# Optimization experiments

Measured on AMD Instinct MI355X. Metric: run time of the kernel, lower is better.

The kernel has to match this reference:

```python
import jax, jax.numpy as jnp
import numpy as np

D_MODEL = 1024
EXPANSION = 4
NUM_TILES = 4
D_FF = D_MODEL * EXPANSION


def setup_inputs() -> dict:
    key = jax.random.key(0)
    k1, k2, k3, k4, k5 = jax.random.split(key, 5)
    x = jax.random.normal(k1, (8, 2048, D_MODEL), dtype=jnp.float32)
    w_up = jax.random.normal(k2, (D_FF, D_MODEL), dtype=jnp.float32) * 0.02
    b_up = jax.random.normal(k3, (D_FF,), dtype=jnp.float32) * 0.02
    w_down = jax.random.normal(k4, (D_MODEL, D_FF), dtype=jnp.float32) * 0.02
    b_down = jax.random.normal(k5, (D_MODEL,), dtype=jnp.float32) * 0.02
    return {"x": x, "w_up": w_up, "b_up": b_up, "w_down": w_down, "b_down": b_down}


def reference(x, w_up, b_up, w_down, b_down):
    B, T, C = x.shape
    xf = x.reshape(B * T, C)  # [N, d_model]
    N = B * T

    # Emergent tile signatures: sign of per-tile row sums of up_proj weight.
    tile_up = D_FF // NUM_TILES
    signatures = jnp.sign(w_up.reshape(NUM_TILES, tile_up, C).sum(axis=1))  # [num_tiles, d_model]

    # Routing: argmax over input-signature alignment -> one-hot gate.
    scores = xf @ signatures.T                      # [N, num_tiles]
    winner = jnp.argmax(scores, axis=-1)            # [N]
    gate = jax.nn.one_hot(winner, NUM_TILES, dtype=xf.dtype)  # [N, num_tiles]

    # Tile-gated up projection (gate scales output tile blocks), then ReLU.
    hidden = xf @ w_up.T + b_up                     # [N, d_ff]
    hidden = (hidden.reshape(N, NUM_TILES, tile_up) * gate[:, :, None]).reshape(N, D_FF)
    hidden = jax.nn.relu(hidden)

    # Tile-gated down projection.
    tile_down = D_MODEL // NUM_TILES
    out = hidden @ w_down.T + b_down                # [N, d_model]
    out = (out.reshape(N, NUM_TILES, tile_down) * gate[:, :, None]).reshape(N, D_MODEL)

    return out.reshape(B, T, D_MODEL), gate.reshape(B, T, NUM_TILES)
```

## Files before the change

kernel.cpp:

```cpp
#include <hip/hip_runtime.h>
#include <stdint.h>
#include <stddef.h>

#define N_TOK 16384
#define DM    1024
#define DFF   4096
#define NT    4
#define TU    1024
#define TD    256

typedef __attribute__((ext_vector_type(8))) short  short8;
typedef __attribute__((ext_vector_type(4))) short  short4v;
typedef __attribute__((ext_vector_type(4))) float  floatx4;

__device__ inline unsigned short f2bf(float f){
  union { float f; uint32_t u; } v; v.f = f;
  uint32_t u = v.u + 0x7FFFu + ((v.u >> 16) & 1u);
  return (unsigned short)(u >> 16);
}

__device__ __forceinline__ void gll16(const void* g, void* l){
  __builtin_amdgcn_global_load_lds(
      (const __attribute__((address_space(1))) unsigned int*)g,
      (__attribute__((address_space(3))) unsigned int*)l,
      16, 0, 0);
}

__global__ void k_sig_partial(const float* __restrict__ w_up,
                              float* __restrict__ partial,
                              unsigned short* __restrict__ wupb){
  const int b = blockIdx.x, tid = threadIdx.x;
  const int tile = b >> 6, chunk = b & 63;
  const int c0 = tid * 4;
  const int row0 = tile*TU + chunk*16;
  float s0=0.f, s1=0.f, s2=0.f, s3=0.f;
  const float* base = w_up + (size_t)row0 * DM + c0;
  #pragma unroll
  for (int r = 0; r < 16; ++r){
    floatx4 v = *(const floatx4*)(base + (size_t)r * DM);
    s0 += v[0]; s1 += v[1]; s2 += v[2]; s3 += v[3];
    short4v p;
    p[0]=(short)f2bf(v[0]); p[1]=(short)f2bf(v[1]);
    p[2]=(short)f2bf(v[2]); p[3]=(short)f2bf(v[3]);
    *(short4v*)(wupb + (size_t)(row0 + r) * DM + c0) = p;
  }
  float* p = partial + ((size_t)tile*DM + c0) * 64 + chunk;
  p[0] = s0; p[64] = s1; p[128] = s2; p[192] = s3;
}

__global__ void k_sig_final(const float* __restrict__ partial,
                            float* __restrict__ sig){
  const int g = blockIdx.x * 256 + threadIdx.x;
  const float* p = partial + (size_t)g * 64;
  float s = 0.f;
  #pragma unroll
  for (int i = 0; i < 64; ++i) s += p[i];
  sig[g] = (s > 0.f) ? 1.f : ((s < 0.f) ? -1.f : 0.f);
}

__global__ void k_wdown_conv(const float* __restrict__ w,
                             unsigned short* __restrict__ wb){
  const size_t i = ((size_t)blockIdx.x * 256 + threadIdx.x) * 8;
  floatx4 v0 = *(const floatx4*)(w + i);
  floatx4 v1 = *(const floatx4*)(w + i + 4);
  short8 p;
  p[0]=(short)f2bf(v0[0]); p[1]=(short)f2bf(v0[1]); p[2]=(short)f2bf(v0[2]); p[3]=(short)f2bf(v0[3]);
  p[4]=(short)f2bf(v1[0]); p[5]=(short)f2bf(v1[1]); p[6]=(short)f2bf(v1[2]); p[7]=(short)f2bf(v1[3]);
  *(short8*)(wb + i) = p;
}

__global__ __launch_bounds__(256) void k_route(
    const float* __restrict__ x, const float* __restrict__ sig,
    float* __restrict__ gate_out, int* __restrict__ winner,
    unsigned short* __restrict__ xbf){
  __shared__ float ssig[NT * DM];
  const int tid = threadIdx.x;
  for (int i = tid; i < NT*DM; i += 256) ssig[i] = sig[i];
  __syncthreads();
  const int wv = tid >> 6, lane = tid & 63;
  const int n = blockIdx.x * 4 + wv;
  const float* xr = x + (size_t)n * DM;
  unsigned short* xb = xbf + (size_t)n * 2048 + 1024;
  double a0=0.0, a1=0.0, a2=0.0, a3=0.0;
  #pragma unroll
  for (int j = 0; j < 4; ++j){
    const int c = j*256 + lane*4;
    floatx4 v = *(const floatx4*)(xr + c);
    short4v p;
    p[0]=(short)f2bf(v[0]); p[1]=(short)f2bf(v[1]);
    p[2]=(short)f2bf(v[2]); p[3]=(short)f2bf(v[3]);
    *(short4v*)(xb + c) = p;
    #pragma unroll
    for (int u = 0; u < 4; ++u){
      double xv = (double)v[u];
      a0 += xv * (double)ssig[c+u];
      a1 += xv * (double)ssig[DM   + c+u];
      a2 += xv * (double)ssig[2*DM + c+u];
      a3 += xv * (double)ssig[3*DM + c+u];
    }
  }
  #pragma unroll
  for (int off = 32; off > 0; off >>= 1){
    a0 += __shfl_down(a0, off, 64);
    a1 += __shfl_down(a1, off, 64);
    a2 += __shfl_down(a2, off, 64);
    a3 += __shfl_down(a3, off, 64);
  }
  if (lane == 0){
    double s[4] = {a0, a1, a2, a3};
    int w = 0;
    #pragma unroll
    for (int t = 1; t < 4; ++t) if (s[t] > s[w]) w = t;
    floatx4 g = { w==0 ? 1.f:0.f, w==1 ? 1.f:0.f, w==2 ? 1.f:0.f, w==3 ? 1.f:0.f };
    *(floatx4*)(gate_out + (size_t)n * 4) = g;
    winner[n] = w;
  }
}

__global__ void k_hist(const int* __restrict__ winner,
                       int* __restrict__ blk_cnt){
  __shared__ int wcnt[4][NT];
  const int tid = threadIdx.x, wv = tid >> 6, lane = tid & 63;
  const int w = winner[blockIdx.x * 256 + tid];
  #pragma unroll
  for (int t = 0; t < NT; ++t){
    unsigned long long m = __ballot(w == t);
    if (lane == 0) wcnt[wv][t] = __popcll(m);
  }
  __syncthreads();
  if (tid < NT){
    int s = wcnt[0][tid] + wcnt[1][tid] + wcnt[2][tid] + wcnt[3][tid];
    blk_cnt[blockIdx.x * NT + tid] = s;
  }
}

__global__ void k_scan(const int* __restrict__ blk_cnt,
                       int* __restrict__ meta, int* __restrict__ blk_base){
  __shared__ int s[256];
  const int tid = threadIdx.x;
  s[tid] = blk_cnt[tid];
  __syncthreads();
  if (tid == 0){
    int tot[NT] = {0,0,0,0};
    for (int b = 0; b < 64; ++b)
      for (int t = 0; t < NT; ++t) tot[t] += s[b*NT + t];
    int off = 0, base[NT];
    for (int t = 0; t < NT; ++t){ meta[t] = tot[t]; meta[4+t] = off; base[t] = off; off += tot[t]; }
    for (int b = 0; b < 64; ++b)
      for (int t = 0; t < NT; ++t){ int c = s[b*NT + t]; s[b*NT + t] = base[t]; base[t] += c; }
  }
  __syncthreads();
  blk_base[tid] = s[tid];
}

__global__ void k_scatter(const int* __restrict__ winner,
                          const int* __restrict__ blk_base,
                          int* __restrict__ idx){
  __shared__ int wcnt[4][NT];
  const int tid = threadIdx.x, wv = tid >> 6, lane = tid & 63;
  const int n = blockIdx.x * 256 + tid;
  const int w = winner[n];
  unsigned long long mymask = 0;
  #pragma unroll
  for (int t = 0; t < NT; ++t){
    unsigned long long m = __ballot(w == t);
    if (lane == 0) wcnt[wv][t] = __popcll(m);
    if (t == w) mymask = m;
  }
  __syncthreads();
  const unsigned long long below = (lane == 0) ? 0ull : (~0ull >> (64 - lane));
  int pos = blk_base[blockIdx.x * NT + w] + __popcll(mymask & below);
  for (int v = 0; v < wv; ++v) pos += wcnt[v][w];
  idx[pos] = n;
}

__global__ __launch_bounds__(256, 2) void k_gemm1(
    const unsigned short* __restrict__ xbf,
    const unsigned short* __restrict__ wupb,
    const float* __restrict__ b_up, const int* __restrict__ meta,
    const int* __restrict__ idx, unsigned short* __restrict__ hid){
  const int tile = blockIdx.z;
  const int cnt  = meta[tile];
  const int p0   = blockIdx.x * 128;
  if (p0 >= cnt) return;
  const int off  = meta[4 + tile];
  const int nb   = blockIdx.y;

  __shared__ unsigned short smem[16384];
  unsigned short* As0 = smem;
  unsigned short* As1 = smem + 4096;
  unsigned short* Bs0 = smem + 8192;
  unsigned short* Bs1 = smem + 12288;
  __shared__ int nrow[128];

  const int tid = threadIdx.x;
  if (tid < 128){
    int p = p0 + tid;
    nrow[tid] = idx[off + (p < cnt ? p : cnt - 1)];
  }
  __syncthreads();

  const int wv = tid >> 6, lane = tid & 63;
  const int wm = (wv >> 1) * 64, wn = (wv & 1) * 64;
  const int l16 = lane & 15, quad = lane >> 4;

  const int rsub = lane >> 2;
  const int kus  = (lane & 3) * 8;

  const int ra = wv*32 + rsub;
  const unsigned short* aptr0 = xbf + (size_t)nrow[ra]      * 2048 + 1024 + kus;
  const unsigned short* aptr1 = xbf + (size_t)nrow[ra + 16] * 2048 + 1024 + kus;
  const unsigned short* bptr0 = wupb + (size_t)(tile*TU + nb*128 + wv*32 + rsub) * DM + kus;
  const unsigned short* bptr1 = bptr0 + 16 * DM;

  unsigned short* a0d0 = As0 + (wv*32) * 32;  unsigned short* a0d1 = a0d0 + 16*32;
  unsigned short* a1d0 = As1 + (wv*32) * 32;  unsigned short* a1d1 = a1d0 + 16*32;
  unsigned short* b0d0 = Bs0 + (wv*32) * 32;  unsigned short* b0d1 = b0d0 + 16*32;
  unsigned short* b1d0 = Bs1 + (wv*32) * 32;  unsigned short* b1d1 = b1d0 + 16*32;

  floatx4 acc[4][4];
  #pragma unroll
  for (int i = 0; i < 4; ++i)
    #pragma unroll
    for (int j = 0; j < 4; ++j) acc[i][j] = (floatx4){0.f,0.f,0.f,0.f};

  for (int k0 = 0; k0 < DM; k0 += 64){
    gll16(aptr0 + k0,      a0d0);
    gll16(aptr1 + k0,      a0d1);
    gll16(aptr0 + k0 + 32, a1d0);
    gll16(aptr1 + k0 + 32, a1d1);
    gll16(bptr0 + k0,      b0d0);
    gll16(bptr1 + k0,      b0d1);
    gll16(bptr0 + k0 + 32, b1d0);
    gll16(bptr1 + k0 + 32, b1d1);
    __syncthreads();
    {
      short8 af[4], bfr[4];
      #pragma unroll
      for (int i = 0; i < 4; ++i) af[i]  = *(const short8*)(As0 + (wm + i*16 + l16)*32 + quad*8);
      #pragma unroll
      for (int j = 0; j < 4; ++j) bfr[j] = *(const short8*)(Bs0 + (wn + j*16 + l16)*32 + quad*8);
      #pragma unroll
      for (int i = 0; i < 4; ++i)
        #pragma unroll
        for (int j = 0; j < 4; ++j)
          acc[i][j] = __builtin_amdgcn_mfma_f32_16x16x32_bf16(af[i], bfr[j], acc[i][j], 0, 0, 0);
    }
    {
      short8 af[4], bfr[4];
      #pragma unroll
      for (int i = 0; i < 4; ++i) af[i]  = *(const short8*)(As1 + (wm + i*16 + l16)*32 + quad*8);
      #pragma unroll
      for (int j = 0; j < 4; ++j) bfr[j] = *(const short8*)(Bs1 + (wn + j*16 + l16)*32 + quad*8);
      #pragma unroll
      for (int i = 0; i < 4; ++i)
        #pragma unroll
        for (int j = 0; j < 4; ++j)
          acc[i][j] = __builtin_amdgcn_mfma_f32_16x16x32_bf16(af[i], bfr[j], acc[i][j], 0, 0, 0);
    }
    __syncthreads();
  }

  const int gcol0 = nb*128;
  #pragma unroll
  for (int half = 0; half < 2; ++half){
    if ((wv >> 1) == half){
      #pragma unroll
      for (int i = 0; i < 4; ++i){
        #pragma unroll
        for (int j = 0; j < 4; ++j){
          const int col = wn + j*16 + l16;
          const float bias = b_up[tile*TU + gcol0 + col];
          #pragma unroll
          for (int r = 0; r < 4; ++r){
            const int lrow = i*16 + quad*4 + r;
            float v = acc[i][j][r] + bias;
            smem[lrow*136 + col] = f2bf(v > 0.f ? v : 0.f);
          }
        }
      }
    }
    __syncthreads();
    #pragma unroll
    for (int c = tid; c < 1024; c += 256){
      const int lrow = c >> 4, k8 = (c & 15) * 8;
      const int m = half*64 + lrow;
      if (p0 + m < cnt){
        short8 vv = *(const short8*)(smem + lrow*136 + k8);
        *(short8*)(hid + (size_t)nrow[m]*2048 + gcol0 + k8) = vv;
      }
    }
    __syncthreads();
  }
}

__global__ __launch_bounds__(256, 2) void k_gemm2(
    const unsigned short* __restrict__ hid,
    const unsigned short* __restrict__ wdownb,
    const float* __restrict__ b_down, const int* __restrict__ meta,
    const int* __restrict__ idx, float* __restrict__ out){
  const int tile = blockIdx.z;
  const int cnt  = meta[tile];
  const int p0   = blockIdx.x * 32;
  if (p0 >= cnt) return;
  const int off  = meta[4 + tile];

  __shared__ unsigned short smem[18432];
  unsigned short* As0 = smem;
  unsigned short* As1 = smem + 1024;
  unsigned short* Bs0 = smem + 2048;
  unsigned short* Bs1 = smem + 10240;
  float* epi = (float*)smem;
  __shared__ int nrow[32];

  const int tid = threadIdx.x;
  if (tid < 32){
    int p = p0 + tid;
    nrow[tid] = idx[off + (p < cnt ? p : cnt - 1)];
  }
  __syncthreads();

  const int wv = tid >> 6, lane = tid & 63;
  const int wn = wv * 64;
  const int l16 = lane & 15, quad = lane >> 4;

  const int rsub = lane >> 2;
  const int kus  = (lane & 3) * 8;

  const int arow = (wv & 1)*16 + rsub;
  const unsigned short* aptr = hid + (size_t)nrow[arow] * 2048 + kus;
  const int aoff = (wv >> 1) * 32;
  unsigned short* asd = (wv < 2 ? As0 : As1) + ((wv & 1)*16) * 32;
  const unsigned short* bptr = wdownb + (size_t)(tile*TD + wv*64 + rsub) * DFF + tile*TU + kus;
  unsigned short* bsd0 = Bs0 + (wv*64) * 32;
  unsigned short* bsd1 = Bs1 + (wv*64) * 32;

  floatx4 acc[2][4];
  #pragma unroll
  for (int i = 0; i < 2; ++i)
    #pragma unroll
    for (int j = 0; j < 4; ++j) acc[i][j] = (floatx4){0.f,0.f,0.f,0.f};

  for (int k0 = 0; k0 < TU; k0 += 64){
    gll16(aptr + k0 + aoff, asd);
    gll16(bptr + k0,               bsd0);
    gll16(bptr + k0 + 16*DFF,      bsd0 + 16*32);
    gll16(bptr + k0 + 32*DFF,      bsd0 + 32*32);
    gll16(bptr + k0 + 48*DFF,      bsd0 + 48*32);
    gll16(bptr + k0 + 32,          bsd1);
    gll16(bptr + k0 + 32 + 16*DFF, bsd1 + 16*32);
    gll16(bptr + k0 + 32 + 32*DFF, bsd1 + 32*32);
    gll16(bptr + k0 + 32 + 48*DFF, bsd1 + 48*32);
    __syncthreads();
    {
      short8 af[2], bfr[4];
      #pragma unroll
      for (int i = 0; i < 2; ++i) af[i]  = *(const short8*)(As0 + (i*16 + l16)*32 + quad*8);
      #pragma unroll
      for (int j = 0; j < 4; ++j) bfr[j] = *(const short8*)(Bs0 + (wn + j*16 + l16)*32 + quad*8);
      #pragma unroll
      for (int i = 0; i < 2; ++i)
        #pragma unroll
        for (int j = 0; j < 4; ++j)
          acc[i][j] = __builtin_amdgcn_mfma_f32_16x16x32_bf16(af[i], bfr[j], acc[i][j], 0, 0, 0);
    }
    {
      short8 af[2], bfr[4];
      #pragma unroll
      for (int i = 0; i < 2; ++i) af[i]  = *(const short8*)(As1 + (i*16 + l16)*32 + quad*8);
      #pragma unroll
      for (int j = 0; j < 4; ++j) bfr[j] = *(const short8*)(Bs1 + (wn + j*16 + l16)*32 + quad*8);
      #pragma unroll
      for (int i = 0; i < 2; ++i)
        #pragma unroll
        for (int j = 0; j < 4; ++j)
          acc[i][j] = __builtin_amdgcn_mfma_f32_16x16x32_bf16(af[i], bfr[j], acc[i][j], 0, 0, 0);
    }
    __syncthreads();
  }

  const floatx4 z4 = {0.f, 0.f, 0.f, 0.f};
  #pragma unroll
  for (int cb = 0; cb < 4; ++cb){
    if (cb == tile) continue;
    for (int c = tid; c < 32*64; c += 256){
      const int rowl = c >> 6, c4 = (c & 63) * 4;
      if (p0 + rowl < cnt)
        *(floatx4*)(out + (size_t)nrow[rowl]*DM + cb*256 + c4) = z4;
    }
  }

  #pragma unroll
  for (int half = 0; half < 2; ++half){
    #pragma unroll
    for (int j = 0; j < 4; ++j){
      const int col = wn + j*16 + l16;
      const float bias = b_down[tile*TD + col];
      #pragma unroll
      for (int r = 0; r < 4; ++r){
        const int lrow = quad*4 + r;
        epi[lrow*260 + col] = acc[half][j][r] + bias;
      }
    }
    __syncthreads();
    #pragma unroll
    for (int c = tid; c < 1024; c += 256){
      const int lrow = c >> 6, c4 = (c & 63) * 4;
      const int m = half*16 + lrow;
      if (p0 + m < cnt){
        floatx4 v = *(const floatx4*)(epi + lrow*260 + c4);
        *(floatx4*)(out + (size_t)nrow[m]*DM + tile*TD + c4) = v;
      }
    }
    __syncthreads();
  }
}

extern "C" void kernel_launch(void* const* d_in, const int* in_sizes, int n_in,
                              void* d_out, int out_size, void* d_ws, size_t ws_size,
                              hipStream_t stream){
  const float* x      = (const float*)d_in[0];
  const float* w_up   = (const float*)d_in[1];
  const float* b_up   = (const float*)d_in[2];
  const float* w_down = (const float*)d_in[3];
  const float* b_down = (const float*)d_in[4];

  unsigned short* wupb   = (unsigned short*)d_ws;
  unsigned short* wdownb = wupb + (size_t)DFF * DM;
  float* partial = (float*)(wdownb + (size_t)DM * DFF);
  float* sig     = partial + 262144;
  int*   ints    = (int*)(sig + 4096);
  int*   winner   = ints;
  int*   idx      = ints + 16384;
  int*   meta     = ints + 32768;
  int*   blk_cnt  = ints + 32776;
  int*   blk_base = ints + 33032;

  float*          out  = (float*)d_out;
  float*          gate = out + (size_t)N_TOK * DM;
  unsigned short* ob16 = (unsigned short*)d_out;

  k_sig_partial<<<dim3(NT*64), 256, 0, stream>>>(w_up, partial, wupb);
  k_sig_final  <<<dim3(16),    256, 0, stream>>>(partial, sig);
  k_wdown_conv <<<dim3(2048),  256, 0, stream>>>(w_down, wdownb);
  k_route      <<<dim3(N_TOK/4), 256, 0, stream>>>(x, sig, gate, winner, ob16);
  k_hist       <<<dim3(64),    256, 0, stream>>>(winner, blk_cnt);
  k_scan       <<<dim3(1),     256, 0, stream>>>(blk_cnt, meta, blk_base);
  k_scatter    <<<dim3(64),    256, 0, stream>>>(winner, blk_base, idx);
  k_gemm1      <<<dim3(128, 8, NT), 256, 0, stream>>>(ob16, wupb, b_up, meta, idx, ob16);
  k_gemm2      <<<dim3(512, 1, NT), 256, 0, stream>>>(ob16, wdownb, b_down, meta, idx, out);
}
```

Measured before the change: 273.5 us.

## Double-buffer LDS tiles in both GEMM kernels to overlap loads with MFMA

Both grouped GEMM kernels move from a load-sync-compute-sync loop to a two-stage ping-pong pipeline. The next K-slice is issued with global_load_lds into the second LDS buffer while MFMAs run on the current one. A manual vmcnt wait and s_barrier replace __syncthreads. This is meant to hide global-load latency, and in exchange it doubles LDS use (64KB and 72KB per block), which can lower occupancy below the two blocks per CU that launch_bounds targets.

```diff
diff --git a/kernel.cpp b/kernel.cpp
--- a/kernel.cpp
+++ b/kernel.cpp
@@ -186,11 +186,7 @@
   const int off  = meta[4 + tile];
   const int nb   = blockIdx.y;
 
-  __shared__ unsigned short smem[16384];
-  unsigned short* As0 = smem;
-  unsigned short* As1 = smem + 4096;
-  unsigned short* Bs0 = smem + 8192;
-  unsigned short* Bs1 = smem + 12288;
+  __shared__ unsigned short smem[32768];
   __shared__ int nrow[128];
 
   const int tid = threadIdx.x;
@@ -213,10 +209,7 @@
   const unsigned short* bptr0 = wupb + (size_t)(tile*TU + nb*128 + wv*32 + rsub) * DM + kus;
   const unsigned short* bptr1 = bptr0 + 16 * DM;
 
-  unsigned short* a0d0 = As0 + (wv*32) * 32;  unsigned short* a0d1 = a0d0 + 16*32;
-  unsigned short* a1d0 = As1 + (wv*32) * 32;  unsigned short* a1d1 = a1d0 + 16*32;
-  unsigned short* b0d0 = Bs0 + (wv*32) * 32;  unsigned short* b0d1 = b0d0 + 16*32;
-  unsigned short* b1d0 = Bs1 + (wv*32) * 32;  unsigned short* b1d1 = b1d0 + 16*32;
+  unsigned short* d0 = smem + (wv*32) * 32;
 
   floatx4 acc[4][4];
   #pragma unroll
@@ -224,22 +217,27 @@
     #pragma unroll
     for (int j = 0; j < 4; ++j) acc[i][j] = (floatx4){0.f,0.f,0.f,0.f};
 
-  for (int k0 = 0; k0 < DM; k0 += 64){
-    gll16(aptr0 + k0,      a0d0);
-    gll16(aptr1 + k0,      a0d1);
-    gll16(aptr0 + k0 + 32, a1d0);
-    gll16(aptr1 + k0 + 32, a1d1);
-    gll16(bptr0 + k0,      b0d0);
-    gll16(bptr1 + k0,      b0d1);
-    gll16(bptr0 + k0 + 32, b1d0);
-    gll16(bptr1 + k0 + 32, b1d1);
-    __syncthreads();
+  auto stage = [&](int B, int k0){
+    unsigned short* d = d0 + B*16384;
+    gll16(aptr0 + k0,      d);
+    gll16(aptr1 + k0,      d + 512);
+    gll16(aptr0 + k0 + 32, d + 4096);
+    gll16(aptr1 + k0 + 32, d + 4608);
+    gll16(bptr0 + k0,      d + 8192);
+    gll16(bptr1 + k0,      d + 8704);
+    gll16(bptr0 + k0 + 32, d + 12288);
+    gll16(bptr1 + k0 + 32, d + 12800);
+  };
+
+  auto compute = [&](int B){
+    const unsigned short* A  = smem + B*16384;
+    const unsigned short* Bp = A + 8192;
     {
       short8 af[4], bfr[4];
       #pragma unroll
-      for (int i = 0; i < 4; ++i) af[i]  = *(const short8*)(As0 + (wm + i*16 + l16)*32 + quad*8);
-      #pragma unroll
-      for (int j = 0; j < 4; ++j) bfr[j] = *(const short8*)(Bs0 + (wn + j*16 + l16)*32 + quad*8);
+      for (int i = 0; i < 4; ++i) af[i]  = *(const short8*)(A  + (wm + i*16 + l16)*32 + quad*8);
+      #pragma unroll
+      for (int j = 0; j < 4; ++j) bfr[j] = *(const short8*)(Bp + (wn + j*16 + l16)*32 + quad*8);
       #pragma unroll
       for (int i = 0; i < 4; ++i)
         #pragma unroll
@@ -249,16 +247,30 @@
     {
       short8 af[4], bfr[4];
       #pragma unroll
-      for (int i = 0; i < 4; ++i) af[i]  = *(const short8*)(As1 + (wm + i*16 + l16)*32 + quad*8);
-      #pragma unroll
-      for (int j = 0; j < 4; ++j) bfr[j] = *(const short8*)(Bs1 + (wn + j*16 + l16)*32 + quad*8);
+      for (int i = 0; i < 4; ++i) af[i]  = *(const short8*)(A  + 4096 + (wm + i*16 + l16)*32 + quad*8);
+      #pragma unroll
+      for (int j = 0; j < 4; ++j) bfr[j] = *(const short8*)(Bp + 4096 + (wn + j*16 + l16)*32 + quad*8);
       #pragma unroll
       for (int i = 0; i < 4; ++i)
         #pragma unroll
         for (int j = 0; j < 4; ++j)
           acc[i][j] = __builtin_amdgcn_mfma_f32_16x16x32_bf16(af[i], bfr[j], acc[i][j], 0, 0, 0);
     }
-    __syncthreads();
+  };
+
+  stage(0, 0);
+  asm volatile("s_waitcnt vmcnt(0)" ::: "memory");
+  __builtin_amdgcn_s_barrier();
+
+  for (int it = 0; it < 16; it += 2){
+    stage(1, (it+1)*64);
+    compute(0);
+    asm volatile("s_waitcnt vmcnt(0)" ::: "memory");
+    __builtin_amdgcn_s_barrier();
+    if (it < 14) stage(0, (it+2)*64);
+    compute(1);
+    asm volatile("s_waitcnt vmcnt(0)" ::: "memory");
+    __builtin_amdgcn_s_barrier();
   }
 
   const int gcol0 = nb*128;
@@ -305,11 +317,7 @@
   if (p0 >= cnt) return;
   const int off  = meta[4 + tile];
 
-  __shared__ unsigned short smem[18432];
-  unsigned short* As0 = smem;
-  unsigned short* As1 = smem + 1024;
-  unsigned short* Bs0 = smem + 2048;
-  unsigned short* Bs1 = smem + 10240;
+  __shared__ unsigned short smem[36864];
   float* epi = (float*)smem;
   __shared__ int nrow[32];
 
@@ -330,10 +338,10 @@
   const int arow = (wv & 1)*16 + rsub;
   const unsigned short* aptr = hid + (size_t)nrow[arow] * 2048 + kus;
   const int aoff = (wv >> 1) * 32;
-  unsigned short* asd = (wv < 2 ? As0 : As1) + ((wv & 1)*16) * 32;
+  unsigned short* asd0 = smem + (wv < 2 ? 0 : 1024) + ((wv & 1)*16) * 32;
   const unsigned short* bptr = wdownb + (size_t)(tile*TD + wv*64 + rsub) * DFF + tile*TU + kus;
-  unsigned short* bsd0 = Bs0 + (wv*64) * 32;
-  unsigned short* bsd1 = Bs1 + (wv*64) * 32;
+  unsigned short* bsd0 = smem + 2048  + (wv*64) * 32;
+  unsigned short* bsd1 = smem + 10240 + (wv*64) * 32;
 
   floatx4 acc[2][4];
   #pragma unroll
@@ -341,23 +349,29 @@
     #pragma unroll
     for (int j = 0; j < 4; ++j) acc[i][j] = (floatx4){0.f,0.f,0.f,0.f};
 
-  for (int k0 = 0; k0 < TU; k0 += 64){
-    gll16(aptr + k0 + aoff, asd);
-    gll16(bptr + k0,               bsd0);
-    gll16(bptr + k0 + 16*DFF,      bsd0 + 16*32);
-    gll16(bptr + k0 + 32*DFF,      bsd0 + 32*32);
-    gll16(bptr + k0 + 48*DFF,      bsd0 + 48*32);
-    gll16(bptr + k0 + 32,          bsd1);
-    gll16(bptr + k0 + 32 + 16*DFF, bsd1 + 16*32);
-    gll16(bptr + k0 + 32 + 32*DFF, bsd1 + 32*32);
-    gll16(bptr + k0 + 32 + 48*DFF, bsd1 + 48*32);
-    __syncthreads();
+  auto stage = [&](int B, int k0){
+    unsigned short* a  = asd0 + B*18432;
+    unsigned short* b0 = bsd0 + B*18432;
+    unsigned short* b1 = bsd1 + B*18432;
+    gll16(aptr + k0 + aoff,        a);
+    gll16(bptr + k0,               b0);
+    gll16(bptr + k0 + 16*DFF,      b0 + 512);
+    gll16(bptr + k0 + 32*DFF,      b0 + 1024);
+    gll16(bptr + k0 + 48*DFF,      b0 + 1536);
+    gll16(bptr + k0 + 32,          b1);
+    gll16(bptr + k0 + 32 + 16*DFF, b1 + 512);
+    gll16(bptr + k0 + 32 + 32*DFF, b1 + 1024);
+    gll16(bptr + k0 + 32 + 48*DFF, b1 + 1536);
+  };
+
+  auto compute = [&](int B){
+    const unsigned short* base = smem + B*18432;
     {
       short8 af[2], bfr[4];
       #pragma unroll
-      for (int i = 0; i < 2; ++i) af[i]  = *(const short8*)(As0 + (i*16 + l16)*32 + quad*8);
-      #pragma unroll
-      for (int j = 0; j < 4; ++j) bfr[j] = *(const short8*)(Bs0 + (wn + j*16 + l16)*32 + quad*8);
+      for (int i = 0; i < 2; ++i) af[i]  = *(const short8*)(base + (i*16 + l16)*32 + quad*8);
+      #pragma unroll
+      for (int j = 0; j < 4; ++j) bfr[j] = *(const short8*)(base + 2048 + (wn + j*16 + l16)*32 + quad*8);
       #pragma unroll
       for (int i = 0; i < 2; ++i)
         #pragma unroll
@@ -367,16 +381,30 @@
     {
       short8 af[2], bfr[4];
       #pragma unroll
-      for (int i = 0; i < 2; ++i) af[i]  = *(const short8*)(As1 + (i*16 + l16)*32 + quad*8);
-      #pragma unroll
-      for (int j = 0; j < 4; ++j) bfr[j] = *(const short8*)(Bs1 + (wn + j*16 + l16)*32 + quad*8);
+      for (int i = 0; i < 2; ++i) af[i]  = *(const short8*)(base + 1024 + (i*16 + l16)*32 + quad*8);
+      #pragma unroll
+      for (int j = 0; j < 4; ++j) bfr[j] = *(const short8*)(base + 10240 + (wn + j*16 + l16)*32 + quad*8);
       #pragma unroll
       for (int i = 0; i < 2; ++i)
         #pragma unroll
         for (int j = 0; j < 4; ++j)
           acc[i][j] = __builtin_amdgcn_mfma_f32_16x16x32_bf16(af[i], bfr[j], acc[i][j], 0, 0, 0);
     }
-    __syncthreads();
+  };
+
+  stage(0, 0);
+  asm volatile("s_waitcnt vmcnt(0)" ::: "memory");
+  __builtin_amdgcn_s_barrier();
+
+  for (int it = 0; it < 16; it += 2){
+    stage(1, (it+1)*64);
+    compute(0);
+    asm volatile("s_waitcnt vmcnt(0)" ::: "memory");
+    __builtin_amdgcn_s_barrier();
+    if (it < 14) stage(0, (it+2)*64);
+    compute(1);
+    asm volatile("s_waitcnt vmcnt(0)" ::: "memory");
+    __builtin_amdgcn_s_barrier();
   }
 
   const floatx4 z4 = {0.f, 0.f, 0.f, 0.f};
```

Result: slower. 291.3 us (+6.5%).

## Triple-buffer GEMM1 LDS loads with vmcnt-based async prefetch pipeline

Applied to the files above, without the earlier changes.

Replaces the load-sync-compute-sync loop in the up-projection GEMM with a 3-stage ring buffer in LDS. Global-to-LDS loads for stage s+2 are issued before computing stage s, and explicit s_waitcnt vmcnt tracks completion so loads overlap the MFMA work. This hides memory latency at the cost of more LDS per block (48KB vs 32KB), which may limit occupancy, and adds a fully unrolled loop of 32 iterations.

```diff
diff --git a/kernel.cpp b/kernel.cpp
--- a/kernel.cpp
+++ b/kernel.cpp
@@ -186,11 +186,7 @@
   const int off  = meta[4 + tile];
   const int nb   = blockIdx.y;
 
-  __shared__ unsigned short smem[16384];
-  unsigned short* As0 = smem;
-  unsigned short* As1 = smem + 4096;
-  unsigned short* Bs0 = smem + 8192;
-  unsigned short* Bs1 = smem + 12288;
+  __shared__ unsigned short smem[24576];
   __shared__ int nrow[128];
 
   const int tid = threadIdx.x;
@@ -213,52 +209,50 @@
   const unsigned short* bptr0 = wupb + (size_t)(tile*TU + nb*128 + wv*32 + rsub) * DM + kus;
   const unsigned short* bptr1 = bptr0 + 16 * DM;
 
-  unsigned short* a0d0 = As0 + (wv*32) * 32;  unsigned short* a0d1 = a0d0 + 16*32;
-  unsigned short* a1d0 = As1 + (wv*32) * 32;  unsigned short* a1d1 = a1d0 + 16*32;
-  unsigned short* b0d0 = Bs0 + (wv*32) * 32;  unsigned short* b0d1 = b0d0 + 16*32;
-  unsigned short* b1d0 = Bs1 + (wv*32) * 32;  unsigned short* b1d1 = b1d0 + 16*32;
-
   floatx4 acc[4][4];
   #pragma unroll
   for (int i = 0; i < 4; ++i)
     #pragma unroll
     for (int j = 0; j < 4; ++j) acc[i][j] = (floatx4){0.f,0.f,0.f,0.f};
 
-  for (int k0 = 0; k0 < DM; k0 += 64){
-    gll16(aptr0 + k0,      a0d0);
-    gll16(aptr1 + k0,      a0d1);
-    gll16(aptr0 + k0 + 32, a1d0);
-    gll16(aptr1 + k0 + 32, a1d1);
-    gll16(bptr0 + k0,      b0d0);
-    gll16(bptr1 + k0,      b0d1);
-    gll16(bptr0 + k0 + 32, b1d0);
-    gll16(bptr1 + k0 + 32, b1d1);
-    __syncthreads();
-    {
-      short8 af[4], bfr[4];
-      #pragma unroll
-      for (int i = 0; i < 4; ++i) af[i]  = *(const short8*)(As0 + (wm + i*16 + l16)*32 + quad*8);
-      #pragma unroll
-      for (int j = 0; j < 4; ++j) bfr[j] = *(const short8*)(Bs0 + (wn + j*16 + l16)*32 + quad*8);
-      #pragma unroll
-      for (int i = 0; i < 4; ++i)
-        #pragma unroll
-        for (int j = 0; j < 4; ++j)
-          acc[i][j] = __builtin_amdgcn_mfma_f32_16x16x32_bf16(af[i], bfr[j], acc[i][j], 0, 0, 0);
-    }
-    {
-      short8 af[4], bfr[4];
-      #pragma unroll
-      for (int i = 0; i < 4; ++i) af[i]  = *(const short8*)(As1 + (wm + i*16 + l16)*32 + quad*8);
-      #pragma unroll
-      for (int j = 0; j < 4; ++j) bfr[j] = *(const short8*)(Bs1 + (wn + j*16 + l16)*32 + quad*8);
-      #pragma unroll
-      for (int i = 0; i < 4; ++i)
-        #pragma unroll
-        for (int j = 0; j < 4; ++j)
-          acc[i][j] = __builtin_amdgcn_mfma_f32_16x16x32_bf16(af[i], bfr[j], acc[i][j], 0, 0, 0);
-    }
-    __syncthreads();
+  auto stage = [&](int b, int s){
+    unsigned short* d = smem + b*8192 + wv*1024;
+    const int ko = s*32;
+    gll16(aptr0 + ko, d);
+    gll16(aptr1 + ko, d + 512);
+    gll16(bptr0 + ko, d + 4096);
+    gll16(bptr1 + ko, d + 4608);
+  };
+
+  auto compute = [&](int b){
+    const unsigned short* A  = smem + b*8192;
+    const unsigned short* Bp = A + 4096;
+    short8 af[4], bfr[4];
+    #pragma unroll
+    for (int i = 0; i < 4; ++i) af[i]  = *(const short8*)(A  + (wm + i*16 + l16)*32 + quad*8);
+    #pragma unroll
+    for (int j = 0; j < 4; ++j) bfr[j] = *(const short8*)(Bp + (wn + j*16 + l16)*32 + quad*8);
+    #pragma unroll
+    for (int i = 0; i < 4; ++i)
+      #pragma unroll
+      for (int j = 0; j < 4; ++j)
+        acc[i][j] = __builtin_amdgcn_mfma_f32_16x16x32_bf16(af[i], bfr[j], acc[i][j], 0, 0, 0);
+  };
+
+  stage(0, 0);
+  stage(1, 1);
+
+  #pragma unroll
+  for (int s = 0; s < 32; ++s){
+    if (s == 31) asm volatile("s_waitcnt vmcnt(0)" ::: "memory");
+    else         asm volatile("s_waitcnt vmcnt(4)" ::: "memory");
+    __builtin_amdgcn_s_barrier();
+    __builtin_amdgcn_sched_barrier(0);
+    if (s < 30) stage((s + 2) % 3, s + 2);
+    compute(s % 3);
+    __builtin_amdgcn_sched_barrier(0);
+    asm volatile("" ::: "memory");
+    __builtin_amdgcn_s_barrier();
   }
 
   const int gcol0 = nb*128;
```

Measured after the change: 276.9 us. Within noise of the previous version (+1.3%).

## Double-buffer LDS in down-proj GEMM and amortize signature loads in routing

Applied to the files above, without the earlier changes.

The down-projection GEMM now uses two LDS buffers, issuing the async global-to-LDS loads for the next K step before computing on the current one. This hides load latency behind MFMA work, at the cost of doubling shared memory per block, which may reduce occupancy. The routing kernel now handles 16 tokens per block and keeps the signature vectors in registers, so fewer blocks reload the signatures into LDS and per-token LDS reads are removed. That raises register pressure.

```diff
diff --git a/kernel.cpp b/kernel.cpp
--- a/kernel.cpp
+++ b/kernel.cpp
@@ -78,42 +78,55 @@
   for (int i = tid; i < NT*DM; i += 256) ssig[i] = sig[i];
   __syncthreads();
   const int wv = tid >> 6, lane = tid & 63;
-  const int n = blockIdx.x * 4 + wv;
-  const float* xr = x + (size_t)n * DM;
-  unsigned short* xb = xbf + (size_t)n * 2048 + 1024;
-  double a0=0.0, a1=0.0, a2=0.0, a3=0.0;
+
+  floatx4 sg[4][4];
   #pragma unroll
   for (int j = 0; j < 4; ++j){
     const int c = j*256 + lane*4;
-    floatx4 v = *(const floatx4*)(xr + c);
-    short4v p;
-    p[0]=(short)f2bf(v[0]); p[1]=(short)f2bf(v[1]);
-    p[2]=(short)f2bf(v[2]); p[3]=(short)f2bf(v[3]);
-    *(short4v*)(xb + c) = p;
-    #pragma unroll
-    for (int u = 0; u < 4; ++u){
-      double xv = (double)v[u];
-      a0 += xv * (double)ssig[c+u];
-      a1 += xv * (double)ssig[DM   + c+u];
-      a2 += xv * (double)ssig[2*DM + c+u];
-      a3 += xv * (double)ssig[3*DM + c+u];
-    }
-  }
-  #pragma unroll
-  for (int off = 32; off > 0; off >>= 1){
-    a0 += __shfl_down(a0, off, 64);
-    a1 += __shfl_down(a1, off, 64);
-    a2 += __shfl_down(a2, off, 64);
-    a3 += __shfl_down(a3, off, 64);
-  }
-  if (lane == 0){
-    double s[4] = {a0, a1, a2, a3};
-    int w = 0;
-    #pragma unroll
-    for (int t = 1; t < 4; ++t) if (s[t] > s[w]) w = t;
-    floatx4 g = { w==0 ? 1.f:0.f, w==1 ? 1.f:0.f, w==2 ? 1.f:0.f, w==3 ? 1.f:0.f };
-    *(floatx4*)(gate_out + (size_t)n * 4) = g;
-    winner[n] = w;
+    #pragma unroll
+    for (int tt = 0; tt < 4; ++tt)
+      sg[j][tt] = *(const floatx4*)(ssig + tt*DM + c);
+  }
+
+  #pragma unroll
+  for (int t = 0; t < 4; ++t){
+    const int n = blockIdx.x * 16 + wv * 4 + t;
+    const float* xr = x + (size_t)n * DM;
+    unsigned short* xb = xbf + (size_t)n * 2048 + 1024;
+    double a0=0.0, a1=0.0, a2=0.0, a3=0.0;
+    #pragma unroll
+    for (int j = 0; j < 4; ++j){
+      const int c = j*256 + lane*4;
+      floatx4 v = *(const floatx4*)(xr + c);
+      short4v p;
+      p[0]=(short)f2bf(v[0]); p[1]=(short)f2bf(v[1]);
+      p[2]=(short)f2bf(v[2]); p[3]=(short)f2bf(v[3]);
+      *(short4v*)(xb + c) = p;
+      #pragma unroll
+      for (int u = 0; u < 4; ++u){
+        double xv = (double)v[u];
+        a0 += xv * (double)sg[j][0][u];
+        a1 += xv * (double)sg[j][1][u];
+        a2 += xv * (double)sg[j][2][u];
+        a3 += xv * (double)sg[j][3][u];
+      }
+    }
+    #pragma unroll
+    for (int off = 32; off > 0; off >>= 1){
+      a0 += __shfl_down(a0, off, 64);
+      a1 += __shfl_down(a1, off, 64);
+      a2 += __shfl_down(a2, off, 64);
+      a3 += __shfl_down(a3, off, 64);
+    }
+    if (lane == 0){
+      double s[4] = {a0, a1, a2, a3};
+      int w = 0;
+      #pragma unroll
+      for (int tt = 1; tt < 4; ++tt) if (s[tt] > s[w]) w = tt;
+      floatx4 g = { w==0 ? 1.f:0.f, w==1 ? 1.f:0.f, w==2 ? 1.f:0.f, w==3 ? 1.f:0.f };
+      *(floatx4*)(gate_out + (size_t)n * 4) = g;
+      winner[n] = w;
+    }
   }
 }
 
@@ -305,11 +318,7 @@
   if (p0 >= cnt) return;
   const int off  = meta[4 + tile];
 
-  __shared__ unsigned short smem[18432];
-  unsigned short* As0 = smem;
-  unsigned short* As1 = smem + 1024;
-  unsigned short* Bs0 = smem + 2048;
-  unsigned short* Bs1 = smem + 10240;
+  __shared__ unsigned short smem[36864];
   float* epi = (float*)smem;
   __shared__ int nrow[32];
 
@@ -330,10 +339,10 @@
   const int arow = (wv & 1)*16 + rsub;
   const unsigned short* aptr = hid + (size_t)nrow[arow] * 2048 + kus;
   const int aoff = (wv >> 1) * 32;
-  unsigned short* asd = (wv < 2 ? As0 : As1) + ((wv & 1)*16) * 32;
+  unsigned short* const asd  = smem + (wv < 2 ? 0 : 1024) + ((wv & 1)*16) * 32;
   const unsigned short* bptr = wdownb + (size_t)(tile*TD + wv*64 + rsub) * DFF + tile*TU + kus;
-  unsigned short* bsd0 = Bs0 + (wv*64) * 32;
-  unsigned short* bsd1 = Bs1 + (wv*64) * 32;
+  unsigned short* const bsd0 = smem + 2048  + (wv*64) * 32;
+  unsigned short* const bsd1 = smem + 10240 + (wv*64) * 32;
 
   floatx4 acc[2][4];
   #pragma unroll
@@ -341,23 +350,29 @@
     #pragma unroll
     for (int j = 0; j < 4; ++j) acc[i][j] = (floatx4){0.f,0.f,0.f,0.f};
 
-  for (int k0 = 0; k0 < TU; k0 += 64){
-    gll16(aptr + k0 + aoff, asd);
-    gll16(bptr + k0,               bsd0);
-    gll16(bptr + k0 + 16*DFF,      bsd0 + 16*32);
-    gll16(bptr + k0 + 32*DFF,      bsd0 + 32*32);
-    gll16(bptr + k0 + 48*DFF,      bsd0 + 48*32);
-    gll16(bptr + k0 + 32,          bsd1);
-    gll16(bptr + k0 + 32 + 16*DFF, bsd1 + 16*32);
-    gll16(bptr + k0 + 32 + 32*DFF, bsd1 + 32*32);
-    gll16(bptr + k0 + 32 + 48*DFF, bsd1 + 48*32);
-    __syncthreads();
+  auto stage = [&](int B, int k0){
+    unsigned short* a  = asd  + B*18432;
+    unsigned short* b0 = bsd0 + B*18432;
+    unsigned short* b1 = bsd1 + B*18432;
+    gll16(aptr + k0 + aoff,        a);
+    gll16(bptr + k0,               b0);
+    gll16(bptr + k0 + 16*DFF,      b0 + 512);
+    gll16(bptr + k0 + 32*DFF,      b0 + 1024);
+    gll16(bptr + k0 + 48*DFF,      b0 + 1536);
+    gll16(bptr + k0 + 32,          b1);
+    gll16(bptr + k0 + 32 + 16*DFF, b1 + 512);
+    gll16(bptr + k0 + 32 + 32*DFF, b1 + 1024);
+    gll16(bptr + k0 + 32 + 48*DFF, b1 + 1536);
+  };
+
+  auto compute = [&](int B){
+    const unsigned short* base = smem + B*18432;
     {
       short8 af[2], bfr[4];
       #pragma unroll
-      for (int i = 0; i < 2; ++i) af[i]  = *(const short8*)(As0 + (i*16 + l16)*32 + quad*8);
-      #pragma unroll
-      for (int j = 0; j < 4; ++j) bfr[j] = *(const short8*)(Bs0 + (wn + j*16 + l16)*32 + quad*8);
+      for (int i = 0; i < 2; ++i) af[i]  = *(const short8*)(base + (i*16 + l16)*32 + quad*8);
+      #pragma unroll
+      for (int j = 0; j < 4; ++j) bfr[j] = *(const short8*)(base + 2048 + (wn + j*16 + l16)*32 + quad*8);
       #pragma unroll
       for (int i = 0; i < 2; ++i)
         #pragma unroll
@@ -367,15 +382,26 @@
     {
       short8 af[2], bfr[4];
       #pragma unroll
-      for (int i = 0; i < 2; ++i) af[i]  = *(const short8*)(As1 + (i*16 + l16)*32 + quad*8);
-      #pragma unroll
-      for (int j = 0; j < 4; ++j) bfr[j] = *(const short8*)(Bs1 + (wn + j*16 + l16)*32 + quad*8);
+      for (int i = 0; i < 2; ++i) af[i]  = *(const short8*)(base + 1024 + (i*16 + l16)*32 + quad*8);
+      #pragma unroll
+      for (int j = 0; j < 4; ++j) bfr[j] = *(const short8*)(base + 10240 + (wn + j*16 + l16)*32 + quad*8);
       #pragma unroll
       for (int i = 0; i < 2; ++i)
         #pragma unroll
         for (int j = 0; j < 4; ++j)
           acc[i][j] = __builtin_amdgcn_mfma_f32_16x16x32_bf16(af[i], bfr[j], acc[i][j], 0, 0, 0);
     }
+  };
+
+  stage(0, 0);
+  __syncthreads();
+
+  for (int it = 0; it < 16; it += 2){
+    stage(1, (it+1)*64);
+    compute(0);
+    __syncthreads();
+    if (it < 14) stage(0, (it+2)*64);
+    compute(1);
     __syncthreads();
   }
 
@@ -443,7 +469,7 @@
   k_sig_partial<<<dim3(NT*64), 256, 0, stream>>>(w_up, partial, wupb);
   k_sig_final  <<<dim3(16),    256, 0, stream>>>(partial, sig);
   k_wdown_conv <<<dim3(2048),  256, 0, stream>>>(w_down, wdownb);
-  k_route      <<<dim3(N_TOK/4), 256, 0, stream>>>(x, sig, gate, winner, ob16);
+  k_route      <<<dim3(N_TOK/16), 256, 0, stream>>>(x, sig, gate, winner, ob16);
   k_hist       <<<dim3(64),    256, 0, stream>>>(winner, blk_cnt);
   k_scan       <<<dim3(1),     256, 0, stream>>>(blk_cnt, meta, blk_base);
   k_scatter    <<<dim3(64),    256, 0, stream>>>(winner, blk_base, idx);
```

Measured after the change: 276.9 us. About the same (+1.3%).
